# Optimization experiments

Measured on AMD Instinct MI355X. Metric: run time of the kernel, lower is better.

Reference implementation:

```python
import jax, jax.numpy as jnp
import numpy as np

N = 100000        # nodes
E = 1600000       # directed edges
F = 602           # Reddit num_features
D = 32            # EMBEDDING_SIZE
C = 41            # Reddit num_classes
BN_EPS = 1e-5


def setup_inputs() -> dict:
    key = jax.random.key(0)
    ks = jax.random.split(key, 24)
    def w(k, shape, fan_in):
        return jax.random.normal(k, shape, dtype=jnp.float32) * (1.0 / np.sqrt(fan_in))
    inp = {
        "x": jax.random.normal(ks[0], (N, F), dtype=jnp.float32),
        "edge_index": jax.random.randint(ks[1], (2, E), 0, N, dtype=jnp.int32),
        # lin1: F -> 2*D
        "lin1_w": w(ks[2], (F, 2 * D), F), "lin1_b": jnp.zeros((2 * D,), jnp.float32),
        # conv1 MLP: 2*D -> D -> D
        "nn1_w1": w(ks[3], (2 * D, D), 2 * D), "nn1_b1": jnp.zeros((D,), jnp.float32),
        "nn1_w2": w(ks[4], (D, D), D), "nn1_b2": jnp.zeros((D,), jnp.float32),
        "bn1_g": jnp.ones((D,), jnp.float32), "bn1_b": jnp.zeros((D,), jnp.float32),
        # conv2 MLP: D -> D -> D
        "nn2_w1": w(ks[5], (D, D), D), "nn2_b1": jnp.zeros((D,), jnp.float32),
        "nn2_w2": w(ks[6], (D, D), D), "nn2_b2": jnp.zeros((D,), jnp.float32),
        "bn2_g": jnp.ones((D,), jnp.float32), "bn2_b": jnp.zeros((D,), jnp.float32),
        # heads
        "fc1_w": w(ks[7], (D, D), D), "fc1_b": jnp.zeros((D,), jnp.float32),
        "fc2_w": w(ks[8], (D, C), D), "fc2_b": jnp.zeros((C,), jnp.float32),
    }
    return inp


def _gin_conv(x, src, dst, w1, b1, w2, b2, eps=0.0):
    # sum-aggregate neighbor features (adj_t @ x) then MLP
    agg = jax.ops.segment_sum(x[src], dst, num_segments=N)  # [N, d]
    h = (1.0 + eps) * x + agg
    h = jnp.maximum(h @ w1 + b1, 0.0) @ w2 + b2
    return h


def _batch_norm(x, gamma, beta):
    # training-mode BatchNorm1d: batch statistics, biased variance
    mu = jnp.mean(x, axis=0)
    var = jnp.mean(jnp.square(x - mu), axis=0)
    return (x - mu) * jax.lax.rsqrt(var + BN_EPS) * gamma + beta


def reference(x, edge_index, lin1_w, lin1_b,
              nn1_w1, nn1_b1, nn1_w2, nn1_b2, bn1_g, bn1_b,
              nn2_w1, nn2_b1, nn2_w2, nn2_b2, bn2_g, bn2_b,
              fc1_w, fc1_b, fc2_w, fc2_b):
    src, dst = edge_index[0], edge_index[1]
    h = x @ lin1_w + lin1_b                                  # [N, 64]
    h = _batch_norm(_gin_conv(h, src, dst, nn1_w1, nn1_b1, nn1_w2, nn1_b2), bn1_g, bn1_b)
    h = _batch_norm(_gin_conv(h, src, dst, nn2_w1, nn2_b1, nn2_w2, nn2_b2), bn2_g, bn2_b)
    h = jnp.maximum(h @ fc1_w + fc1_b, 0.0)
    return h @ fc2_w + fc2_b                                 # [N, C]
```

## Files before the change

kernel.cpp:

```cpp
#include <hip/hip_runtime.h>
#include <cstdint>

#define NN 100000
#define NE 1600000
#define FI 602
#define DD 32
#define CC 41
#define BN_EPS 1e-5f
#define KSTEPS 19

#define NPB 256
#define NB 391
#define BST 4608
#define EPT 13
#define SCB 481

typedef __attribute__((ext_vector_type(8))) short bf16x8;
typedef __attribute__((ext_vector_type(4))) float f32x4;

__device__ __forceinline__ void atomAdd(float* p, float v) {
#ifdef __HIP_PLATFORM_AMD__
  unsafeAtomicAdd(p, v);
#else
  atomicAdd(p, v);
#endif
}

__device__ __forceinline__ unsigned short f2b(float f) {
  unsigned u = __float_as_uint(f);
  unsigned r = (u + 0x7fffu + ((u >> 16) & 1u)) >> 16;
  return (unsigned short)r;
}
__device__ __forceinline__ float blo(unsigned u) { return __uint_as_float(u << 16); }
__device__ __forceinline__ float bhi(unsigned u) { return __uint_as_float(u & 0xffff0000u); }

__global__ __launch_bounds__(256) void k0_prep(
    const float* __restrict__ lin1_w, const float* __restrict__ lin1_b,
    const float* __restrict__ nn1_w1,
    unsigned short* __restrict__ Bh,
    float* __restrict__ cvec,
    float* __restrict__ stats1, float* __restrict__ stats2) {
  int o = blockIdx.x * 256 + threadIdx.x;
  if (o < KSTEPS * 32 * 32) {
    int k = o >> 5, j = o & 31;
    float s = 0.f;
    if (k < FI) {
      #pragma unroll 4
      for (int c = 0; c < 2 * DD; ++c) s = fmaf(lin1_w[k * (2 * DD) + c], nn1_w1[c * DD + j], s);
    }
    int st = k >> 5, kk = k & 31, g = kk >> 3, jj = kk & 7;
    int h = j >> 4, lane = g * 16 + (j & 15);
    int idx = ((st * 2 + h) * 64 + lane) * 8 + jj;
    Bh[idx] = f2b(s);
  }
  if (blockIdx.x == 0) {
    int t = threadIdx.x;
    if (t < DD) {
      float s = 0.f;
      for (int c = 0; c < 2 * DD; ++c) s = fmaf(lin1_b[c], nn1_w1[c * DD + t], s);
      cvec[t] = s;
    }
    if (t >= 128 && t < 192) stats1[t - 128] = 0.f;
    if (t >= 192) stats2[t - 192] = 0.f;
  }
}

__global__ __launch_bounds__(256) void kb_scatter(const int* __restrict__ ei,
                                                  int* __restrict__ bcursor,
                                                  int* __restrict__ tsrc,
                                                  unsigned char* __restrict__ tdst) {
  __shared__ int cnt[NB];
  __shared__ int wbase[NB];
  const int t = threadIdx.x;
  for (int i = t; i < NB; i += 256) cnt[i] = 0;
  __syncthreads();
  const int base = blockIdx.x * (256 * EPT);
  int s[EPT], d[EPT];
  #pragma unroll
  for (int i = 0; i < EPT; ++i) {
    int e = base + i * 256 + t;
    if (e < NE) {
      s[i] = ei[e];
      d[i] = ei[NE + e];
      atomicAdd(&cnt[d[i] >> 8], 1);
    } else {
      s[i] = -1; d[i] = -1;
    }
  }
  __syncthreads();
  for (int i = t; i < NB; i += 256) wbase[i] = atomicAdd(&bcursor[i], cnt[i]);
  __syncthreads();
  #pragma unroll
  for (int i = 0; i < EPT; ++i) {
    if (d[i] >= 0) {
      int bk = d[i] >> 8;
      int p = atomicAdd(&wbase[bk], 1);
      int gp = bk * BST + p;
      tsrc[gp] = s[i];
      tdst[gp] = (unsigned char)(d[i] & (NPB - 1));
    }
  }
}

__global__ __launch_bounds__(256) void kb_fine(const int* __restrict__ bcursor,
                                               const int* __restrict__ tsrc,
                                               const unsigned char* __restrict__ tdst,
                                               int* __restrict__ rs, int* __restrict__ re,
                                               int* __restrict__ srcidx) {
  __shared__ int deg[NPB];
  __shared__ int cur[NPB];
  __shared__ int woff[4];
  const int b = blockIdx.x, t = threadIdx.x;
  const int beg = b * BST;
  const int end = beg + bcursor[b];
  deg[t] = 0;
  __syncthreads();
  for (int i = beg + t; i < end; i += 256) atomicAdd(&deg[tdst[i]], 1);
  __syncthreads();
  int v = deg[t];
  int lane = t & 63, wave = t >> 6;
  int inc = v;
  #pragma unroll
  for (int off = 1; off < 64; off <<= 1) {
    int u = __shfl_up(inc, off);
    if (lane >= off) inc += u;
  }
  if (lane == 63) woff[wave] = inc;
  __syncthreads();
  int wadd = 0;
  for (int w = 0; w < wave; ++w) wadd += woff[w];
  int excl = wadd + inc - v;
  int gnode = b * NPB + t;
  if (gnode < NN) {
    rs[gnode] = beg + excl;
    re[gnode] = beg + excl + v;
  }
  cur[t] = beg + excl;
  __syncthreads();
  for (int i = beg + t; i < end; i += 256) {
    int p = atomicAdd(&cur[tdst[i]], 1);
    srcidx[p] = tsrc[i];
  }
}

__global__ __launch_bounds__(256) void k1_mfma(
    const float* __restrict__ x,
    const unsigned short* __restrict__ Bh,
    const float* __restrict__ cvec, unsigned short* __restrict__ zb) {
  const int lane = threadIdx.x & 63;
  const int wid = (blockIdx.x * 256 + threadIdx.x) >> 6;
  const int row0 = wid * 16;
  if (row0 >= NN) return;
  const int g = lane >> 4;
  const int r = row0 + (lane & 15);
  const float* __restrict__ xr = x + (size_t)r * FI + g * 8;
  f32x4 acc0 = {0.f, 0.f, 0.f, 0.f};
  f32x4 acc1 = {0.f, 0.f, 0.f, 0.f};

  float4 a0 = *(const float4*)&xr[0];
  float4 b0 = *(const float4*)&xr[4];
  float4 a1 = *(const float4*)&xr[32];
  float4 b1 = *(const float4*)&xr[36];
  bf16x8 f0c = *(const bf16x8*)&Bh[(size_t)lane * 8];
  bf16x8 f1c = *(const bf16x8*)&Bh[(size_t)lane * 8 + 512];

  #pragma unroll
  for (int s = 0; s < KSTEPS; ++s) {
    float4 ca = a0, cb = b0;
    a0 = a1; b0 = b1;
    if (s + 2 < KSTEPS - 1) {
      a1 = *(const float4*)&xr[(s + 2) * 32];
      b1 = *(const float4*)&xr[(s + 2) * 32 + 4];
    } else if (s + 2 == KSTEPS - 1) {
      if (g == 3) {
        float2 tt = *(const float2*)&xr[18 * 32];
        a1 = make_float4(tt.x, tt.y, 0.f, 0.f);
        b1 = make_float4(0.f, 0.f, 0.f, 0.f);
      } else {
        a1 = *(const float4*)&xr[18 * 32];
        b1 = *(const float4*)&xr[18 * 32 + 4];
      }
    }
    bf16x8 f0n, f1n;
    if (s + 1 < KSTEPS) {
      const size_t fb = ((size_t)((s + 1) * 2) * 64 + lane) * 8;
      f0n = *(const bf16x8*)&Bh[fb];
      f1n = *(const bf16x8*)&Bh[fb + 512];
    }
    bf16x8 ahi, alo;
    {
      float cv0[8] = {ca.x, ca.y, ca.z, ca.w, cb.x, cb.y, cb.z, cb.w};
      #pragma unroll
      for (int j = 0; j < 8; ++j) {
        unsigned ub = __float_as_uint(cv0[j]);
        unsigned short h = (unsigned short)(ub >> 16);
        float hv = __uint_as_float(ub & 0xffff0000u);
        float d = cv0[j] - hv;
        ahi[j] = (short)h;
        alo[j] = (short)(__float_as_uint(d) >> 16);
      }
    }
    acc0 = __builtin_amdgcn_mfma_f32_16x16x32_bf16(ahi, f0c, acc0, 0, 0, 0);
    acc1 = __builtin_amdgcn_mfma_f32_16x16x32_bf16(ahi, f1c, acc1, 0, 0, 0);
    acc0 = __builtin_amdgcn_mfma_f32_16x16x32_bf16(alo, f0c, acc0, 0, 0, 0);
    acc1 = __builtin_amdgcn_mfma_f32_16x16x32_bf16(alo, f1c, acc1, 0, 0, 0);
    if (s + 1 < KSTEPS) { f0c = f0n; f1c = f1n; }
  }
  const int c0 = lane & 15;
  const float cva = cvec[c0], cvb = cvec[16 + c0];
  #pragma unroll
  for (int j = 0; j < 4; ++j) {
    int rr = row0 + g * 4 + j;
    zb[(size_t)rr * DD + c0] = f2b(acc0[j] + cva);
    zb[(size_t)rr * DD + 16 + c0] = f2b(acc1[j] + cvb);
  }
}

__global__ __launch_bounds__(256) void k_gather_b(const int* __restrict__ rs,
                                                  const int* __restrict__ re,
                                                  const int* __restrict__ srcidx,
                                                  const unsigned short* __restrict__ srcb,
                                                  float* __restrict__ agg) {
  int gid = blockIdx.x * 256 + threadIdx.x;
  int n = gid >> 2, q = gid & 3;
  if (n >= NN) return;
  int beg = rs[n], end = re[n];
  float a[8] = {};
  int i = beg;
  for (; i + 4 <= end; i += 4) {
    int s0 = srcidx[i], s1 = srcidx[i + 1], s2 = srcidx[i + 2], s3 = srcidx[i + 3];
    uint4 v0 = *(const uint4*)&srcb[(size_t)s0 * DD + q * 8];
    uint4 v1 = *(const uint4*)&srcb[(size_t)s1 * DD + q * 8];
    uint4 v2 = *(const uint4*)&srcb[(size_t)s2 * DD + q * 8];
    uint4 v3 = *(const uint4*)&srcb[(size_t)s3 * DD + q * 8];
    a[0] += blo(v0.x) + blo(v1.x) + blo(v2.x) + blo(v3.x);
    a[1] += bhi(v0.x) + bhi(v1.x) + bhi(v2.x) + bhi(v3.x);
    a[2] += blo(v0.y) + blo(v1.y) + blo(v2.y) + blo(v3.y);
    a[3] += bhi(v0.y) + bhi(v1.y) + bhi(v2.y) + bhi(v3.y);
    a[4] += blo(v0.z) + blo(v1.z) + blo(v2.z) + blo(v3.z);
    a[5] += bhi(v0.z) + bhi(v1.z) + bhi(v2.z) + bhi(v3.z);
    a[6] += blo(v0.w) + blo(v1.w) + blo(v2.w) + blo(v3.w);
    a[7] += bhi(v0.w) + bhi(v1.w) + bhi(v2.w) + bhi(v3.w);
  }
  for (; i < end; ++i) {
    uint4 v0 = *(const uint4*)&srcb[(size_t)srcidx[i] * DD + q * 8];
    a[0] += blo(v0.x); a[1] += bhi(v0.x);
    a[2] += blo(v0.y); a[3] += bhi(v0.y);
    a[4] += blo(v0.z); a[5] += bhi(v0.z);
    a[6] += blo(v0.w); a[7] += bhi(v0.w);
  }
  float* ap = &agg[(size_t)n * DD + q * 8];
  *(float4*)&ap[0] = make_float4(a[0], a[1], a[2], a[3]);
  *(float4*)&ap[4] = make_float4(a[4], a[5], a[6], a[7]);
}

__global__ __launch_bounds__(256) void k3_mlp1(
    const unsigned short* __restrict__ zb, const float* __restrict__ agg,
    const float* __restrict__ w2, const float* __restrict__ b1, const float* __restrict__ b2,
    unsigned short* __restrict__ g1b, float* __restrict__ stats) {
  __shared__ float us[256][DD + 1];
  __shared__ float w2s[DD][DD];
  __shared__ float ps[4][2 * DD];
  const int tid = threadIdx.x;
  const int n0 = blockIdx.x * 256;
  for (int i = tid; i < DD * DD; i += 256) w2s[i >> 5][i & 31] = w2[i];
  #pragma unroll
  for (int i = 0; i < 16; ++i) {
    int l = tid + i * 256;
    int r = l >> 4, c2 = l & 15;
    float lo = 0.f, hi = 0.f;
    if (n0 + r < NN) {
      size_t gi = (size_t)(n0 + r) * DD + c2 * 2;
      unsigned u = *(const unsigned*)&zb[gi];
      float2 ag = *(const float2*)&agg[gi];
      lo = blo(u) + ag.x;
      hi = bhi(u) + ag.y;
    }
    us[r][c2 * 2] = lo;
    us[r][c2 * 2 + 1] = hi;
  }
  __syncthreads();
  float t[DD];
  #pragma unroll
  for (int k = 0; k < DD; ++k) t[k] = fmaxf(us[tid][k] + b1[k], 0.f);
  float g[DD];
  #pragma unroll
  for (int j = 0; j < DD; ++j) g[j] = b2[j];
  #pragma unroll
  for (int k = 0; k < DD; ++k) {
    float tv = t[k];
    #pragma unroll
    for (int j = 0; j < DD; ++j) g[j] = fmaf(tv, w2s[k][j], g[j]);
  }
  bool valid = (n0 + tid) < NN;
  #pragma unroll
  for (int j = 0; j < DD; ++j) us[tid][j] = g[j];
  int wave = tid >> 6, lane = tid & 63;
  #pragma unroll
  for (int j = 0; j < DD; ++j) {
    float v = valid ? g[j] : 0.f;
    float qq = v * v;
    #pragma unroll
    for (int off = 1; off < 64; off <<= 1) { v += __shfl_xor(v, off); qq += __shfl_xor(qq, off); }
    if (lane == 0) { ps[wave][j] = v; ps[wave][DD + j] = qq; }
  }
  __syncthreads();
  if (tid < 2 * DD)
    atomAdd(&stats[tid], ps[0][tid] + ps[1][tid] + ps[2][tid] + ps[3][tid]);
  #pragma unroll
  for (int i = 0; i < 16; ++i) {
    int l = tid + i * 256;
    int r = l >> 4, c2 = l & 15;
    if (n0 + r < NN) {
      unsigned u = ((unsigned)f2b(us[r][c2 * 2 + 1]) << 16) | (unsigned)f2b(us[r][c2 * 2]);
      *(unsigned*)&g1b[(size_t)(n0 + r) * DD + c2 * 2] = u;
    }
  }
}

__global__ void k3b_bn(const float* __restrict__ stats, const float* __restrict__ gamma,
                       const float* __restrict__ beta, float* __restrict__ bnp) {
  int t = threadIdx.x;
  if (t < DD) {
    float mu = stats[t] * (1.f / NN);
    float var = stats[DD + t] * (1.f / NN) - mu * mu;
    float rsv = rsqrtf(var + BN_EPS) * gamma[t];
    bnp[t] = rsv;
    bnp[DD + t] = beta[t] - mu * rsv;
  }
}

__global__ __launch_bounds__(256) void k6_mlp2(
    const unsigned short* __restrict__ g1b, const float* __restrict__ agg,
    const int* __restrict__ rsA, const int* __restrict__ reA, const float* __restrict__ bnp,
    const float* __restrict__ w1, const float* __restrict__ b1,
    const float* __restrict__ w2, const float* __restrict__ b2,
    float* __restrict__ g2, float* __restrict__ stats) {
  __shared__ float us[256][DD + 1];
  __shared__ float w1s[DD][DD];
  __shared__ float w2s[DD][DD];
  __shared__ float bns[2 * DD];
  __shared__ float ps[4][2 * DD];
  const int tid = threadIdx.x;
  const int n0 = blockIdx.x * 256;
  for (int i = tid; i < DD * DD; i += 256) { w1s[i >> 5][i & 31] = w1[i]; w2s[i >> 5][i & 31] = w2[i]; }
  if (tid < 2 * DD) bns[tid] = bnp[tid];
  const int n = n0 + tid;
  const bool valid = n < NN;
  float degp1 = 1.f;
  if (valid) degp1 = (float)(reA[n] - rsA[n] + 1);
  #pragma unroll
  for (int i = 0; i < 16; ++i) {
    int l = tid + i * 256;
    int r = l >> 4, c2 = l & 15;
    float lo = 0.f, hi = 0.f;
    if (n0 + r < NN) {
      size_t gi = (size_t)(n0 + r) * DD + c2 * 2;
      unsigned u = *(const unsigned*)&g1b[gi];
      float2 ag = *(const float2*)&agg[gi];
      lo = blo(u) + ag.x;
      hi = bhi(u) + ag.y;
    }
    us[r][c2 * 2] = lo;
    us[r][c2 * 2 + 1] = hi;
  }
  __syncthreads();
  float t1[DD];
  #pragma unroll
  for (int j = 0; j < DD; ++j) t1[j] = b1[j];
  #pragma unroll
  for (int k = 0; k < DD; ++k) {
    float uv = fmaf(us[tid][k], bns[k], degp1 * bns[DD + k]);
    #pragma unroll
    for (int j = 0; j < DD; ++j) t1[j] = fmaf(uv, w1s[k][j], t1[j]);
  }
  #pragma unroll
  for (int j = 0; j < DD; ++j) t1[j] = fmaxf(t1[j], 0.f);
  float g[DD];
  #pragma unroll
  for (int j = 0; j < DD; ++j) g[j] = b2[j];
  #pragma unroll
  for (int k = 0; k < DD; ++k) {
    float tv = t1[k];
    #pragma unroll
    for (int j = 0; j < DD; ++j) g[j] = fmaf(tv, w2s[k][j], g[j]);
  }
  #pragma unroll
  for (int j = 0; j < DD; ++j) us[tid][j] = g[j];
  int wave = tid >> 6, lane = tid & 63;
  #pragma unroll
  for (int j = 0; j < DD; ++j) {
    float v = valid ? g[j] : 0.f;
    float qq = v * v;
    #pragma unroll
    for (int off = 1; off < 64; off <<= 1) { v += __shfl_xor(v, off); qq += __shfl_xor(qq, off); }
    if (lane == 0) { ps[wave][j] = v; ps[wave][DD + j] = qq; }
  }
  __syncthreads();
  if (tid < 2 * DD)
    atomAdd(&stats[tid], ps[0][tid] + ps[1][tid] + ps[2][tid] + ps[3][tid]);
  #pragma unroll
  for (int i = 0; i < 32; ++i) {
    int l = tid + i * 256;
    int r = l >> 5, c = l & 31;
    if (n0 + r < NN) g2[(size_t)(n0 + r) * DD + c] = us[r][c];
  }
}

__global__ __launch_bounds__(256) void k7_head(
    const float* __restrict__ g2, const float* __restrict__ stats2,
    const float* __restrict__ bn2_g, const float* __restrict__ bn2_b,
    const float* __restrict__ fc1_w, const float* __restrict__ fc1_b,
    const float* __restrict__ fc2_w, const float* __restrict__ fc2_b,
    float* __restrict__ out) {
  __shared__ float buf[256 * 42];
  __shared__ float fc1s[DD * DD];
  __shared__ float fc2s[DD * CC];
  __shared__ float mu2[DD], rsg2[DD], bet2[DD];
  const int tid = threadIdx.x;
  const int n0 = blockIdx.x * 256;
  if (tid < DD) {
    float mu = stats2[tid] * (1.f / NN);
    float var = stats2[DD + tid] * (1.f / NN) - mu * mu;
    mu2[tid] = mu;
    rsg2[tid] = rsqrtf(var + BN_EPS) * bn2_g[tid];
    bet2[tid] = bn2_b[tid];
  }
  for (int i = tid; i < DD * DD; i += 256) fc1s[i] = fc1_w[i];
  for (int i = tid; i < DD * CC; i += 256) fc2s[i] = fc2_w[i];
  __syncthreads();
  #pragma unroll
  for (int i = 0; i < 32; ++i) {
    int l = tid + i * 256;
    int r = l >> 5, c = l & 31;
    float v = 0.f;
    if (n0 + r < NN) v = (g2[(size_t)(n0 + r) * DD + c] - mu2[c]) * rsg2[c] + bet2[c];
    buf[r * 33 + c] = v;
  }
  __syncthreads();
  float t[DD];
  #pragma unroll
  for (int j = 0; j < DD; ++j) t[j] = fc1_b[j];
  #pragma unroll
  for (int k = 0; k < DD; ++k) {
    float uv = buf[tid * 33 + k];
    #pragma unroll
    for (int j = 0; j < DD; ++j) t[j] = fmaf(uv, fc1s[k * DD + j], t[j]);
  }
  #pragma unroll
  for (int j = 0; j < DD; ++j) t[j] = fmaxf(t[j], 0.f);
  float o[CC];
  #pragma unroll
  for (int j = 0; j < CC; ++j) o[j] = fc2_b[j];
  #pragma unroll
  for (int k = 0; k < DD; ++k) {
    float tv = t[k];
    #pragma unroll
    for (int j = 0; j < CC; ++j) o[j] = fmaf(tv, fc2s[k * CC + j], o[j]);
  }
  __syncthreads();
  #pragma unroll
  for (int j = 0; j < CC; ++j) buf[tid * 42 + j] = o[j];
  __syncthreads();
  for (int i = 0; i < CC; ++i) {
    int l = tid + i * 256;
    int r = l / CC, c = l % CC;
    if (n0 + r < NN) out[(size_t)(n0 + r) * CC + c] = buf[r * 42 + c];
  }
}

extern "C" void kernel_launch(void* const* d_in, const int* in_sizes, int n_in,
                              void* d_out, int out_size, void* d_ws, size_t ws_size,
                              hipStream_t stream) {
  const float* x      = (const float*)d_in[0];
  const int*   ei     = (const int*)d_in[1];
  const float* lin1_w = (const float*)d_in[2];
  const float* lin1_b = (const float*)d_in[3];
  const float* nn1_w1 = (const float*)d_in[4];
  const float* nn1_b1 = (const float*)d_in[5];
  const float* nn1_w2 = (const float*)d_in[6];
  const float* nn1_b2 = (const float*)d_in[7];
  const float* bn1_g  = (const float*)d_in[8];
  const float* bn1_b  = (const float*)d_in[9];
  const float* nn2_w1 = (const float*)d_in[10];
  const float* nn2_b1 = (const float*)d_in[11];
  const float* nn2_w2 = (const float*)d_in[12];
  const float* nn2_b2 = (const float*)d_in[13];
  const float* bn2_g  = (const float*)d_in[14];
  const float* bn2_b  = (const float*)d_in[15];
  const float* fc1_w  = (const float*)d_in[16];
  const float* fc1_b  = (const float*)d_in[17];
  const float* fc2_w  = (const float*)d_in[18];
  const float* fc2_b  = (const float*)d_in[19];
  float* out = (float*)d_out;

  float* ws = (float*)d_ws;
  size_t nd = (size_t)NN * DD;
  float* A      = ws;
  float* B      = ws + nd;
  float* cvec   = ws + 2 * nd;
  float* stats1 = cvec + 32;
  float* bnp1   = stats1 + 64;
  float* stats2 = bnp1 + 96;
  unsigned short* Bh = (unsigned short*)(stats2 + 64);
  int*   rsA      = (int*)(Bh + KSTEPS * 2 * 64 * 8);
  int*   reA      = rsA + NN;
  int*   srcidx   = reA + NN;
  int*   tsrc     = srcidx + (size_t)NB * BST;
  unsigned char* tdst = (unsigned char*)(tsrc + (size_t)NB * BST);
  int*   bcursor  = (int*)(tdst + (size_t)NB * BST);
  unsigned short* fb16 = (unsigned short*)tsrc;

  hipMemsetAsync(bcursor, 0, NB * sizeof(int), stream);
  kb_scatter<<<SCB, 256, 0, stream>>>(ei, bcursor, tsrc, tdst);
  kb_fine<<<NB, 256, 0, stream>>>(bcursor, tsrc, tdst, rsA, reA, srcidx);

  k0_prep<<<(KSTEPS * 32 * 32 + 255) / 256, 256, 0, stream>>>(
      lin1_w, lin1_b, nn1_w1, Bh, cvec, stats1, stats2);
  k1_mfma<<<(NN / 16 + 3) / 4, 256, 0, stream>>>(x, Bh, cvec, fb16);
  k_gather_b<<<(NN * 4 + 255) / 256, 256, 0, stream>>>(rsA, reA, srcidx, fb16, B);
  k3_mlp1<<<(NN + 255) / 256, 256, 0, stream>>>(fb16, B, nn1_w2, nn1_b1, nn1_b2, fb16, stats1);
  k3b_bn<<<1, 64, 0, stream>>>(stats1, bn1_g, bn1_b, bnp1);
  k_gather_b<<<(NN * 4 + 255) / 256, 256, 0, stream>>>(rsA, reA, srcidx, fb16, B);
  k6_mlp2<<<(NN + 255) / 256, 256, 0, stream>>>(fb16, B, rsA, reA, bnp1,
                                                nn2_w1, nn2_b1, nn2_w2, nn2_b2, A, stats2);
  k7_head<<<(NN + 255) / 256, 256, 0, stream>>>(A, stats2, bn2_g, bn2_b, fc1_w, fc1_b, fc2_w, fc2_b, out);
}
```

Before: 277.9 us.

## Split-K the input projection, deepen gather unroll, fold BN finalize into mlp2

The lin1 MFMA kernel now gives each 16-row tile to two waves that split the K dimension in half. The halves are summed through shared memory, which doubles wave-level parallelism and memory concurrency on the 241 MB x read. The neighbor gather now issues 8 independent row loads per iteration to keep more memory requests in flight. The tiny single-block BN finalize kernel is removed and its math is recomputed in each k6_mlp2 block, saving one launch at the cost of redundant per-block arithmetic.

```diff
diff --git a/kernel.cpp b/kernel.cpp
--- a/kernel.cpp
+++ b/kernel.cpp
@@ -147,48 +147,41 @@
     const float* __restrict__ x,
     const unsigned short* __restrict__ Bh,
     const float* __restrict__ cvec, unsigned short* __restrict__ zb) {
-  const int lane = threadIdx.x & 63;
-  const int wid = (blockIdx.x * 256 + threadIdx.x) >> 6;
-  const int row0 = wid * 16;
-  if (row0 >= NN) return;
+  __shared__ float part[2][64][9];
+  const int tid = threadIdx.x;
+  const int lane = tid & 63;
+  const int w = tid >> 6;
+  const int rg = w & 1;
+  const int kh = w >> 1;
+  const int row0 = blockIdx.x * 32 + rg * 16;
   const int g = lane >> 4;
   const int r = row0 + (lane & 15);
   const float* __restrict__ xr = x + (size_t)r * FI + g * 8;
   f32x4 acc0 = {0.f, 0.f, 0.f, 0.f};
   f32x4 acc1 = {0.f, 0.f, 0.f, 0.f};
 
-  float4 a0 = *(const float4*)&xr[0];
-  float4 b0 = *(const float4*)&xr[4];
-  float4 a1 = *(const float4*)&xr[32];
-  float4 b1 = *(const float4*)&xr[36];
-  bf16x8 f0c = *(const bf16x8*)&Bh[(size_t)lane * 8];
-  bf16x8 f1c = *(const bf16x8*)&Bh[(size_t)lane * 8 + 512];
-
-  #pragma unroll
-  for (int s = 0; s < KSTEPS; ++s) {
-    float4 ca = a0, cb = b0;
-    a0 = a1; b0 = b1;
-    if (s + 2 < KSTEPS - 1) {
-      a1 = *(const float4*)&xr[(s + 2) * 32];
-      b1 = *(const float4*)&xr[(s + 2) * 32 + 4];
-    } else if (s + 2 == KSTEPS - 1) {
-      if (g == 3) {
-        float2 tt = *(const float2*)&xr[18 * 32];
-        a1 = make_float4(tt.x, tt.y, 0.f, 0.f);
-        b1 = make_float4(0.f, 0.f, 0.f, 0.f);
-      } else {
-        a1 = *(const float4*)&xr[18 * 32];
-        b1 = *(const float4*)&xr[18 * 32 + 4];
+  if (kh == 0) {
+    float4 a0 = *(const float4*)&xr[0];
+    float4 b0 = *(const float4*)&xr[4];
+    float4 a1 = *(const float4*)&xr[32];
+    float4 b1 = *(const float4*)&xr[36];
+    bf16x8 f0c = *(const bf16x8*)&Bh[(size_t)lane * 8];
+    bf16x8 f1c = *(const bf16x8*)&Bh[(size_t)lane * 8 + 512];
+    #pragma unroll
+    for (int s = 0; s < 10; ++s) {
+      float4 ca = a0, cb = b0;
+      a0 = a1; b0 = b1;
+      if (s + 2 < 10) {
+        a1 = *(const float4*)&xr[(s + 2) * 32];
+        b1 = *(const float4*)&xr[(s + 2) * 32 + 4];
       }
-    }
-    bf16x8 f0n, f1n;
-    if (s + 1 < KSTEPS) {
-      const size_t fb = ((size_t)((s + 1) * 2) * 64 + lane) * 8;
-      f0n = *(const bf16x8*)&Bh[fb];
-      f1n = *(const bf16x8*)&Bh[fb + 512];
-    }
-    bf16x8 ahi, alo;
-    {
+      bf16x8 f0n, f1n;
+      if (s + 1 < 10) {
+        const size_t fb = ((size_t)((s + 1) * 2) * 64 + lane) * 8;
+        f0n = *(const bf16x8*)&Bh[fb];
+        f1n = *(const bf16x8*)&Bh[fb + 512];
+      }
+      bf16x8 ahi, alo;
       float cv0[8] = {ca.x, ca.y, ca.z, ca.w, cb.x, cb.y, cb.z, cb.w};
       #pragma unroll
       for (int j = 0; j < 8; ++j) {
@@ -199,20 +192,77 @@
         ahi[j] = (short)h;
         alo[j] = (short)(__float_as_uint(d) >> 16);
       }
-    }
-    acc0 = __builtin_amdgcn_mfma_f32_16x16x32_bf16(ahi, f0c, acc0, 0, 0, 0);
-    acc1 = __builtin_amdgcn_mfma_f32_16x16x32_bf16(ahi, f1c, acc1, 0, 0, 0);
-    acc0 = __builtin_amdgcn_mfma_f32_16x16x32_bf16(alo, f0c, acc0, 0, 0, 0);
-    acc1 = __builtin_amdgcn_mfma_f32_16x16x32_bf16(alo, f1c, acc1, 0, 0, 0);
-    if (s + 1 < KSTEPS) { f0c = f0n; f1c = f1n; }
-  }
-  const int c0 = lane & 15;
-  const float cva = cvec[c0], cvb = cvec[16 + c0];
-  #pragma unroll
-  for (int j = 0; j < 4; ++j) {
-    int rr = row0 + g * 4 + j;
-    zb[(size_t)rr * DD + c0] = f2b(acc0[j] + cva);
-    zb[(size_t)rr * DD + 16 + c0] = f2b(acc1[j] + cvb);
+      acc0 = __builtin_amdgcn_mfma_f32_16x16x32_bf16(ahi, f0c, acc0, 0, 0, 0);
+      acc1 = __builtin_amdgcn_mfma_f32_16x16x32_bf16(ahi, f1c, acc1, 0, 0, 0);
+      acc0 = __builtin_amdgcn_mfma_f32_16x16x32_bf16(alo, f0c, acc0, 0, 0, 0);
+      acc1 = __builtin_amdgcn_mfma_f32_16x16x32_bf16(alo, f1c, acc1, 0, 0, 0);
+      if (s + 1 < 10) { f0c = f0n; f1c = f1n; }
+    }
+  } else {
+    float4 a0 = *(const float4*)&xr[10 * 32];
+    float4 b0 = *(const float4*)&xr[10 * 32 + 4];
+    float4 a1 = *(const float4*)&xr[11 * 32];
+    float4 b1 = *(const float4*)&xr[11 * 32 + 4];
+    bf16x8 f0c = *(const bf16x8*)&Bh[((size_t)(10 * 2) * 64 + lane) * 8];
+    bf16x8 f1c = *(const bf16x8*)&Bh[((size_t)(10 * 2) * 64 + lane) * 8 + 512];
+    #pragma unroll
+    for (int s = 10; s < KSTEPS; ++s) {
+      float4 ca = a0, cb = b0;
+      a0 = a1; b0 = b1;
+      if (s + 2 < KSTEPS - 1) {
+        a1 = *(const float4*)&xr[(s + 2) * 32];
+        b1 = *(const float4*)&xr[(s + 2) * 32 + 4];
+      } else if (s + 2 == KSTEPS - 1) {
+        if (g == 3) {
+          float2 tt = *(const float2*)&xr[18 * 32];
+          a1 = make_float4(tt.x, tt.y, 0.f, 0.f);
+          b1 = make_float4(0.f, 0.f, 0.f, 0.f);
+        } else {
+          a1 = *(const float4*)&xr[18 * 32];
+          b1 = *(const float4*)&xr[18 * 32 + 4];
+        }
+      }
+      bf16x8 f0n, f1n;
+      if (s + 1 < KSTEPS) {
+        const size_t fb = ((size_t)((s + 1) * 2) * 64 + lane) * 8;
+        f0n = *(const bf16x8*)&Bh[fb];
+        f1n = *(const bf16x8*)&Bh[fb + 512];
+      }
+      bf16x8 ahi, alo;
+      float cv0[8] = {ca.x, ca.y, ca.z, ca.w, cb.x, cb.y, cb.z, cb.w};
+      #pragma unroll
+      for (int j = 0; j < 8; ++j) {
+        unsigned ub = __float_as_uint(cv0[j]);
+        unsigned short h = (unsigned short)(ub >> 16);
+        float hv = __uint_as_float(ub & 0xffff0000u);
+        float d = cv0[j] - hv;
+        ahi[j] = (short)h;
+        alo[j] = (short)(__float_as_uint(d) >> 16);
+      }
+      acc0 = __builtin_amdgcn_mfma_f32_16x16x32_bf16(ahi, f0c, acc0, 0, 0, 0);
+      acc1 = __builtin_amdgcn_mfma_f32_16x16x32_bf16(ahi, f1c, acc1, 0, 0, 0);
+      acc0 = __builtin_amdgcn_mfma_f32_16x16x32_bf16(alo, f0c, acc0, 0, 0, 0);
+      acc1 = __builtin_amdgcn_mfma_f32_16x16x32_bf16(alo, f1c, acc1, 0, 0, 0);
+      if (s + 1 < KSTEPS) { f0c = f0n; f1c = f1n; }
+    }
+    #pragma unroll
+    for (int j = 0; j < 4; ++j) {
+      part[rg][lane][j] = acc0[j];
+      part[rg][lane][4 + j] = acc1[j];
+    }
+  }
+  __syncthreads();
+  if (kh == 0) {
+    const int c0 = lane & 15;
+    const float cva = cvec[c0], cvb = cvec[16 + c0];
+    #pragma unroll
+    for (int j = 0; j < 4; ++j) {
+      float v0 = acc0[j] + part[rg][lane][j] + cva;
+      float v1 = acc1[j] + part[rg][lane][4 + j] + cvb;
+      int rr = row0 + g * 4 + j;
+      zb[(size_t)rr * DD + c0] = f2b(v0);
+      zb[(size_t)rr * DD + 16 + c0] = f2b(v1);
+    }
   }
 }
 
@@ -227,20 +277,29 @@
   int beg = rs[n], end = re[n];
   float a[8] = {};
   int i = beg;
+  for (; i + 8 <= end; i += 8) {
+    uint4 v[8];
+    #pragma unroll
+    for (int j = 0; j < 8; ++j) v[j] = *(const uint4*)&srcb[(size_t)srcidx[i + j] * DD + q * 8];
+    #pragma unroll
+    for (int j = 0; j < 8; ++j) {
+      a[0] += blo(v[j].x); a[1] += bhi(v[j].x);
+      a[2] += blo(v[j].y); a[3] += bhi(v[j].y);
+      a[4] += blo(v[j].z); a[5] += bhi(v[j].z);
+      a[6] += blo(v[j].w); a[7] += bhi(v[j].w);
+    }
+  }
   for (; i + 4 <= end; i += 4) {
-    int s0 = srcidx[i], s1 = srcidx[i + 1], s2 = srcidx[i + 2], s3 = srcidx[i + 3];
-    uint4 v0 = *(const uint4*)&srcb[(size_t)s0 * DD + q * 8];
-    uint4 v1 = *(const uint4*)&srcb[(size_t)s1 * DD + q * 8];
-    uint4 v2 = *(const uint4*)&srcb[(size_t)s2 * DD + q * 8];
-    uint4 v3 = *(const uint4*)&srcb[(size_t)s3 * DD + q * 8];
-    a[0] += blo(v0.x) + blo(v1.x) + blo(v2.x) + blo(v3.x);
-    a[1] += bhi(v0.x) + bhi(v1.x) + bhi(v2.x) + bhi(v3.x);
-    a[2] += blo(v0.y) + blo(v1.y) + blo(v2.y) + blo(v3.y);
-    a[3] += bhi(v0.y) + bhi(v1.y) + bhi(v2.y) + bhi(v3.y);
-    a[4] += blo(v0.z) + blo(v1.z) + blo(v2.z) + blo(v3.z);
-    a[5] += bhi(v0.z) + bhi(v1.z) + bhi(v2.z) + bhi(v3.z);
-    a[6] += blo(v0.w) + blo(v1.w) + blo(v2.w) + blo(v3.w);
-    a[7] += bhi(v0.w) + bhi(v1.w) + bhi(v2.w) + bhi(v3.w);
+    uint4 v[4];
+    #pragma unroll
+    for (int j = 0; j < 4; ++j) v[j] = *(const uint4*)&srcb[(size_t)srcidx[i + j] * DD + q * 8];
+    #pragma unroll
+    for (int j = 0; j < 4; ++j) {
+      a[0] += blo(v[j].x); a[1] += bhi(v[j].x);
+      a[2] += blo(v[j].y); a[3] += bhi(v[j].y);
+      a[4] += blo(v[j].z); a[5] += bhi(v[j].z);
+      a[6] += blo(v[j].w); a[7] += bhi(v[j].w);
+    }
   }
   for (; i < end; ++i) {
     uint4 v0 = *(const uint4*)&srcb[(size_t)srcidx[i] * DD + q * 8];
@@ -318,21 +377,10 @@
   }
 }
 
-__global__ void k3b_bn(const float* __restrict__ stats, const float* __restrict__ gamma,
-                       const float* __restrict__ beta, float* __restrict__ bnp) {
-  int t = threadIdx.x;
-  if (t < DD) {
-    float mu = stats[t] * (1.f / NN);
-    float var = stats[DD + t] * (1.f / NN) - mu * mu;
-    float rsv = rsqrtf(var + BN_EPS) * gamma[t];
-    bnp[t] = rsv;
-    bnp[DD + t] = beta[t] - mu * rsv;
-  }
-}
-
 __global__ __launch_bounds__(256) void k6_mlp2(
     const unsigned short* __restrict__ g1b, const float* __restrict__ agg,
-    const int* __restrict__ rsA, const int* __restrict__ reA, const float* __restrict__ bnp,
+    const int* __restrict__ rsA, const int* __restrict__ reA,
+    const float* __restrict__ stats1, const float* __restrict__ bn1_g, const float* __restrict__ bn1_b,
     const float* __restrict__ w1, const float* __restrict__ b1,
     const float* __restrict__ w2, const float* __restrict__ b2,
     float* __restrict__ g2, float* __restrict__ stats) {
@@ -344,7 +392,13 @@
   const int tid = threadIdx.x;
   const int n0 = blockIdx.x * 256;
   for (int i = tid; i < DD * DD; i += 256) { w1s[i >> 5][i & 31] = w1[i]; w2s[i >> 5][i & 31] = w2[i]; }
-  if (tid < 2 * DD) bns[tid] = bnp[tid];
+  if (tid < DD) {
+    float mu = stats1[tid] * (1.f / NN);
+    float var = stats1[DD + tid] * (1.f / NN) - mu * mu;
+    float rsv = rsqrtf(var + BN_EPS) * bn1_g[tid];
+    bns[tid] = rsv;
+    bns[DD + tid] = bn1_b[tid] - mu * rsv;
+  }
   const int n = n0 + tid;
   const bool valid = n < NN;
   float degp1 = 1.f;
@@ -500,8 +554,7 @@
   float* B      = ws + nd;
   float* cvec   = ws + 2 * nd;
   float* stats1 = cvec + 32;
-  float* bnp1   = stats1 + 64;
-  float* stats2 = bnp1 + 96;
+  float* stats2 = stats1 + 64;
   unsigned short* Bh = (unsigned short*)(stats2 + 64);
   int*   rsA      = (int*)(Bh + KSTEPS * 2 * 64 * 8);
   int*   reA      = rsA + NN;
@@ -517,12 +570,11 @@
 
   k0_prep<<<(KSTEPS * 32 * 32 + 255) / 256, 256, 0, stream>>>(
       lin1_w, lin1_b, nn1_w1, Bh, cvec, stats1, stats2);
-  k1_mfma<<<(NN / 16 + 3) / 4, 256, 0, stream>>>(x, Bh, cvec, fb16);
+  k1_mfma<<<NN / 32, 256, 0, stream>>>(x, Bh, cvec, fb16);
   k_gather_b<<<(NN * 4 + 255) / 256, 256, 0, stream>>>(rsA, reA, srcidx, fb16, B);
   k3_mlp1<<<(NN + 255) / 256, 256, 0, stream>>>(fb16, B, nn1_w2, nn1_b1, nn1_b2, fb16, stats1);
-  k3b_bn<<<1, 64, 0, stream>>>(stats1, bn1_g, bn1_b, bnp1);
   k_gather_b<<<(NN * 4 + 255) / 256, 256, 0, stream>>>(rsA, reA, srcidx, fb16, B);
-  k6_mlp2<<<(NN + 255) / 256, 256, 0, stream>>>(fb16, B, rsA, reA, bnp1,
+  k6_mlp2<<<(NN + 255) / 256, 256, 0, stream>>>(fb16, B, rsA, reA, stats1, bn1_g, bn1_b,
                                                 nn2_w1, nn2_b1, nn2_w2, nn2_b2, A, stats2);
   k7_head<<<(NN + 255) / 256, 256, 0, stream>>>(A, stats2, bn2_g, bn2_b, fc1_w, fc1_b, fc2_w, fc2_b, out);
 }
```

Measured after the change: 269.0 us. -3.2%, faster.
